# Optimization experiments

Measured on AMD Instinct MI355X. Metric: run time of the kernel, lower is better.

The kernel has to match this reference:

```python
import jax, jax.numpy as jnp
import numpy as np

V, E, Hd, ENC, A = 2000, 256, 256, 256, 256
B, HI, WI, T = 64, 16, 32, 256


def setup_inputs() -> dict:
    key = jax.random.key(0)
    ks = jax.random.split(key, 24)
    n = lambda k, s: jax.random.normal(k, s, dtype=jnp.float32) * 0.05
    return {
        "encoder_out": jax.random.normal(ks[0], (B, ENC, HI, WI), dtype=jnp.float32),
        "captions": jax.random.randint(ks[1], (B, T), 0, V),
        "emb": n(ks[2], (V, E)),
        "W_ae": n(ks[3], (A, ENC)), "b_ae": jnp.zeros((A,), jnp.float32),
        "W_ad": n(ks[4], (A, Hd)), "b_ad": jnp.zeros((A,), jnp.float32),
        "W_fa": n(ks[5], (1, A)), "b_fa": jnp.zeros((1,), jnp.float32),
        "W_inith": n(ks[6], (Hd, ENC)), "b_inith": jnp.zeros((Hd,), jnp.float32),
        "W_initc": n(ks[7], (Hd, ENC)), "b_initc": jnp.zeros((Hd,), jnp.float32),
        "W_ih0": n(ks[8], (4 * Hd, E + ENC)), "W_hh0": n(ks[9], (4 * Hd, Hd)),
        "b_ih0": jnp.zeros((4 * Hd,), jnp.float32), "b_hh0": jnp.zeros((4 * Hd,), jnp.float32),
        "W_ih1": n(ks[10], (4 * Hd, Hd)), "W_hh1": n(ks[11], (4 * Hd, Hd)),
        "b_ih1": jnp.zeros((4 * Hd,), jnp.float32), "b_hh1": jnp.zeros((4 * Hd,), jnp.float32),
        "W_out": n(ks[12], (V, Hd)), "b_out": jnp.zeros((V,), jnp.float32),
    }


def _lstm_cell(x, h, c, Wih, Whh, bih, bhh):
    # PyTorch LSTM gate order: i, f, g, o
    g = x @ Wih.T + h @ Whh.T + bih + bhh
    i, f, gg, o = jnp.split(g, 4, axis=-1)
    c2 = jax.nn.sigmoid(f) * c + jax.nn.sigmoid(i) * jnp.tanh(gg)
    h2 = jax.nn.sigmoid(o) * jnp.tanh(c2)
    return h2, c2


def reference(encoder_out, captions, emb, W_ae, b_ae, W_ad, b_ad, W_fa, b_fa,
              W_inith, b_inith, W_initc, b_initc,
              W_ih0, W_hh0, b_ih0, b_hh0, W_ih1, W_hh1, b_ih1, b_hh1,
              W_out, b_out):
    Bsz, C = encoder_out.shape[0], encoder_out.shape[1]
    enc = encoder_out.reshape(Bsz, C, -1).transpose(0, 2, 1)  # [B, P, C]
    mean = encoder_out.mean(axis=(2, 3))                      # [B, C]
    h0 = jnp.tanh(mean @ W_inith.T + b_inith)
    c0 = jnp.tanh(mean @ W_initc.T + b_initc)
    h = jnp.stack([h0, h0])  # [L, B, Hd]
    c = jnp.stack([c0, c0])
    embs = emb[captions]     # [B, T, E] (dropout disabled / eval)
    att1 = enc @ W_ae.T + b_ae  # [B, P, A], hoisted out of the loop (same math)

    def step(carry, e_t):
        h, c = carry
        att2 = h[-1] @ W_ad.T + b_ad                              # [B, A]
        score = (jnp.tanh(att1 + att2[:, None, :]) @ W_fa.T)[..., 0] + b_fa[0]  # [B, P]
        w = jax.nn.softmax(score, axis=1)
        ctx = jnp.einsum('bp,bpc->bc', w, enc)
        x = jnp.concatenate([e_t, ctx], axis=1)                   # [B, E+C]
        h0n, c0n = _lstm_cell(x, h[0], c[0], W_ih0, W_hh0, b_ih0, b_hh0)
        h1n, c1n = _lstm_cell(h0n, h[1], c[1], W_ih1, W_hh1, b_ih1, b_hh1)
        out_t = h1n @ W_out.T + b_out
        return (jnp.stack([h0n, h1n]), jnp.stack([c0n, c1n])), (out_t, w)

    _, (outs, ws) = jax.lax.scan(step, (h, c), embs.transpose(1, 0, 2))
    return outs.transpose(1, 0, 2), ws.transpose(1, 0, 2)  # [B,T,V], [B,T,P]
```

## Files before the change

### kernel.cpp

```cpp
#include <hip/hip_runtime.h>
#include <math.h>

#define BB 64
#define TT 256
#define VV 2000
#define EE 256
#define HD 256
#define ENC 256
#define AA 256
#define PP 512


typedef unsigned uvec4 __attribute__((ext_vector_type(4)));

__device__ __forceinline__ unsigned short f2h(float f) {
    _Float16 h = (_Float16)f; return __builtin_bit_cast(unsigned short, h);
}
__device__ __forceinline__ void fmlo(float& a, unsigned w, float x) {
    asm("v_fma_mix_f32 %0, %1, %2, %0 op_sel_hi:[1,0,0]" : "+v"(a) : "v"(w), "v"(x));
}
__device__ __forceinline__ void fmhi(float& a, unsigned w, float x) {
    asm("v_fma_mix_f32 %0, %1, %2, %0 op_sel:[1,0,0] op_sel_hi:[1,0,0]" : "+v"(a) : "v"(w), "v"(x));
}
__device__ __forceinline__ void dot8m(float& a0, float& a1, uvec4 w, float4 xa, float4 xb) {
    fmlo(a0, w.x, xa.x); fmhi(a1, w.x, xa.y);
    fmlo(a0, w.y, xa.z); fmhi(a1, w.y, xa.w);
    fmlo(a0, w.z, xb.x); fmhi(a1, w.z, xb.y);
    fmlo(a0, w.w, xb.z); fmhi(a1, w.w, xb.w);
}


__global__ void k_mean(const float* __restrict__ enc, float* __restrict__ meanb) {
    int b = blockIdx.x, c = threadIdx.x;
    const float4* p4 = reinterpret_cast<const float4*>(enc + ((size_t)b*ENC + c)*PP);
    float s = 0.f;
    for (int i = 0; i < PP/4; ++i) { float4 v = p4[i]; s += v.x + v.y + v.z + v.w; }
    meanb[b*ENC + c] = s * (1.0f/PP);
}

__global__ void k_init(const float* __restrict__ meanb,
                       const float* __restrict__ Winith, const float* __restrict__ binith,
                       const float* __restrict__ Winitc, const float* __restrict__ binitc,
                       float* __restrict__ h0, float* __restrict__ c0,
                       float* __restrict__ h1i, float* __restrict__ c1) {
    __shared__ float ms[ENC];
    int b = blockIdx.x, j = threadIdx.x;
    ms[j] = meanb[b*ENC + j];
    __syncthreads();
    float ah = binith[j], ac = binitc[j];
    const float4* wh = (const float4*)(Winith + (size_t)j*ENC);
    const float4* wc = (const float4*)(Winitc + (size_t)j*ENC);
    const float4* m4 = (const float4*)ms;
    for (int k = 0; k < ENC/4; ++k) {
        float4 m = m4[k], a = wh[k], b2 = wc[k];
        ah += a.x*m.x + a.y*m.y + a.z*m.z + a.w*m.w;
        ac += b2.x*m.x + b2.y*m.y + b2.z*m.z + b2.w*m.w;
    }
    float hv = tanhf(ah), cv = tanhf(ac);
    h0[b*HD + j] = hv; c0[b*HD + j] = cv;
    h1i[b*HD + j] = hv; c1[b*HD + j] = cv;
}

__global__ void k_att1T8(const float* __restrict__ enc, const float* __restrict__ Wae,
                         const float* __restrict__ bae, unsigned short* __restrict__ att1T8) {
    __shared__ float wsm[16][ENC];
    int a0 = blockIdx.x * 16, b = blockIdx.y, p = threadIdx.x;
    for (int i = threadIdx.x; i < 16*ENC; i += 512) wsm[i >> 8][i & 255] = Wae[(size_t)a0*ENC + i];
    __syncthreads();
    float acc[16];
    #pragma unroll
    for (int i = 0; i < 16; ++i) acc[i] = 0.f;
    const float* eb = enc + (size_t)b*ENC*PP + p;
    for (int c = 0; c < ENC; ++c) {
        float v = eb[(size_t)c*PP];
        #pragma unroll
        for (int i = 0; i < 16; ++i) acc[i] += v * wsm[i][c];
    }
    #pragma unroll
    for (int q = 0; q < 2; ++q) {
        unsigned short o[8];
        #pragma unroll
        for (int j = 0; j < 8; ++j) o[j] = f2h(acc[q*8+j] + bae[a0 + q*8 + j]);
        *(uint4*)(att1T8 + (((size_t)b*32 + (a0 >> 3) + q)*PP + p)*8) = *(const uint4*)o;
    }
}

__global__ void k_encP(const float* __restrict__ enc, unsigned short* __restrict__ encP) {
    __shared__ float tile[256*33];
    int b = blockIdx.x, p0 = blockIdx.y * 32, tid = threadIdx.x;
    for (int i = tid; i < 256*32; i += 256) {
        int c = i >> 5, pl = i & 31;
        tile[c*33 + pl] = enc[((size_t)b*ENC + c)*PP + p0 + pl];
    }
    __syncthreads();
    for (int j = tid; j < 32*256; j += 256) {
        int p = j >> 8, c = j & 255;
        encP[((size_t)b*PP + p0 + p)*ENC + c] = f2h(tile[c*33 + p]);
    }
}

__global__ void k_cvtT8(const float* __restrict__ src, unsigned short* __restrict__ dst,
                        int nsh, int kc) {
    int i = blockIdx.x*256 + threadIdx.x;
    int N = 1 << nsh;
    int kk = i >> nsh, n = i & (N - 1);
    const float* s = src + (size_t)n*(kc*8) + kk*8;
    unsigned short o[8];
    #pragma unroll
    for (int j = 0; j < 8; ++j) o[j] = f2h(s[j]);
    *(uint4*)(dst + ((size_t)kk*N + n)*8) = *(const uint4*)o;
}


struct KP2 {
    const int* caps; const float* emb;
    const float* Wfa; const float* bfa; const float* bad;
    const float* bih0; const float* bhh0; const float* bih1; const float* bhh1;
    const unsigned short* WadT8;
    const unsigned short* Wih0T8;
    const unsigned short* Whh0T8;
    const unsigned short* Wih1T8;
    const unsigned short* Whh1T8;
    const unsigned short* att1T8;
    const unsigned short* encP;
    const float* h0g; const float* c0g; const float* h1g; const float* c1g;
    float* H1all; float* wsout;
};

__global__ __launch_bounds__(1024, 1) void main64(KP2 P) {
    __shared__ float att2s[AA];
    __shared__ float xt[512];
    __shared__ float h0s[HD], h1s[HD];
    __shared__ float es[PP];
    __shared__ float red[2048];
    __shared__ float bs0[1024], bs1[1024];
    __shared__ float badS[AA], wfaS[AA];
    __shared__ float zinvS, bfaS;
    __shared__ int capS;

    const int b = blockIdx.x, tid = threadIdx.x;

    bs0[tid] = P.bih0[tid] + P.bhh0[tid];
    bs1[tid] = P.bih1[tid] + P.bhh1[tid];
    float c0r = 0.f, c1r = 0.f;
    if (tid < 256) {
        badS[tid] = P.bad[tid]; wfaS[tid] = P.Wfa[tid];
        h0s[tid] = P.h0g[b*HD + tid]; h1s[tid] = P.h1g[b*HD + tid];
        c0r = P.c0g[b*HD + tid];      c1r = P.c1g[b*HD + tid];
    }
    if (tid == 0) bfaS = P.bfa[0];
    __syncthreads();

    const uvec4* att1b = (const uvec4*)(P.att1T8 + (size_t)b*32*PP*8);
    const unsigned* encPb = (const unsigned*)(P.encP + (size_t)b*PP*ENC);
    const uvec4* wadt = (const uvec4*)P.WadT8;
    const uvec4* wi0t = (const uvec4*)P.Wih0T8;
    const uvec4* wh0t = (const uvec4*)P.Whh0T8;
    const uvec4* wi1t = (const uvec4*)P.Wih1T8;
    const uvec4* wh1t = (const uvec4*)P.Whh1T8;

    for (int t = 0; t < TT; ++t) {
        {
            int a = tid & 255, kq = tid >> 8;
            const uvec4* w4 = wadt + (size_t)(kq*8)*256 + a;
            const float4* hv = (const float4*)h1s;
            float a0 = 0.f, a1 = 0.f;
            #pragma unroll
            for (int i = 0; i < 8; ++i) {
                uvec4 w = w4[(size_t)i*256];
                dot8m(a0, a1, w, hv[(kq*8 + i)*2], hv[(kq*8 + i)*2 + 1]);
            }
            red[kq*256 + a] = a0 + a1;
        }
        if (tid == 1023) capS = P.caps[b*TT + t];
        __syncthreads();
        if (tid < 256) att2s[tid] = red[tid] + red[256+tid] + red[512+tid] + red[768+tid] + badS[tid];
        __syncthreads();

        {
            int p = tid & 511, h = tid >> 9;
            const uvec4* a4 = att1b + (size_t)(h*16)*PP + p;
            float sc = 0.f;
            float one = 1.0f;
            #pragma unroll 4
            for (int i = 0; i < 16; ++i) {
                uvec4 w = __builtin_nontemporal_load(a4 + (size_t)i*PP);
                int ab = (h*16 + i)*8;
                #pragma unroll
                for (int j = 0; j < 4; ++j) {
                    unsigned wj = w[j];
                    float a2l = att2s[ab + j*2], a2h = att2s[ab + j*2 + 1];
                    float x0, x1;
                    asm("v_fma_mix_f32 %0, %1, %2, %3 op_sel_hi:[1,0,0]"
                        : "=v"(x0) : "v"(wj), "v"(one), "v"(a2l));
                    asm("v_fma_mix_f32 %0, %1, %2, %3 op_sel:[1,0,0] op_sel_hi:[1,0,0]"
                        : "=v"(x1) : "v"(wj), "v"(one), "v"(a2h));
                    float r0 = __builtin_amdgcn_rcpf(__expf(2.f*x0) + 1.f);
                    float r1 = __builtin_amdgcn_rcpf(__expf(2.f*x1) + 1.f);
                    sc += wfaS[ab + j*2]     * (1.f - 2.f*r0)
                        + wfaS[ab + j*2 + 1] * (1.f - 2.f*r1);
                }
            }
            red[h*512 + p] = sc;
        }
        __syncthreads();
        if (tid < 512) es[tid] = __expf(red[tid] + red[512 + tid] + bfaS);
        __syncthreads();

        if (tid < 64) {
            float z = 0.f;
            #pragma unroll
            for (int i = 0; i < 8; ++i) z += es[tid*8 + i];
            for (int o = 32; o > 0; o >>= 1) z += __shfl_down(z, o, 64);
            if (tid == 0) zinvS = 1.f / z;
        }
        {
            int c2 = tid & 127, pq = tid >> 7;
            float a0 = 0.f, a1 = 0.f;
            #pragma unroll 8
            for (int i = 0; i < 64; ++i) {
                int p = pq*64 + i;
                unsigned w = __builtin_nontemporal_load(encPb + (size_t)p*128 + c2);
                float e = es[p];
                fmlo(a0, w, e); fmhi(a1, w, e);
            }
            red[pq*256 + c2*2]     = a0;
            red[pq*256 + c2*2 + 1] = a1;
        }
        __syncthreads();
        if (tid < 256) {
            float s = 0.f;
            #pragma unroll
            for (int q = 0; q < 8; ++q) s += red[q*256 + tid];
            xt[256 + tid] = s * zinvS;
        } else if (tid < 512) {
            int j = tid - 256;
            xt[j] = P.emb[(size_t)capS*EE + j];
        } else {
            int p = tid - 512;
            P.wsout[((size_t)b*TT + t)*PP + p] = es[p] * zinvS;
        }
        __syncthreads();

        {
            float a0 = bs0[tid], a1 = 0.f;
            const uvec4* wi = wi0t + tid;
            const float4* xv = (const float4*)xt;
            #pragma unroll 8
            for (int kk = 0; kk < 64; ++kk) {
                uvec4 w = wi[(size_t)kk*1024];
                dot8m(a0, a1, w, xv[kk*2], xv[kk*2 + 1]);
            }
            const uvec4* wh = wh0t + tid;
            const float4* hv = (const float4*)h0s;
            #pragma unroll 8
            for (int kk = 0; kk < 32; ++kk) {
                uvec4 w = wh[(size_t)kk*1024];
                dot8m(a0, a1, w, hv[kk*2], hv[kk*2 + 1]);
            }
            red[tid] = a0 + a1;
        }
        __syncthreads();
        if (tid < 256) {
            float gi = red[tid], gf = red[HD+tid], gg = red[2*HD+tid], go = red[3*HD+tid];
            float si = 1.f/(1.f + __expf(-gi)), sf = 1.f/(1.f + __expf(-gf)), so = 1.f/(1.f + __expf(-go));
            c0r = sf*c0r + si*tanhf(gg);
            h0s[tid] = so*tanhf(c0r);
        }
        __syncthreads();

        {
            float a0 = bs1[tid], a1 = 0.f;
            const uvec4* wi = wi1t + tid;
            const float4* hv0 = (const float4*)h0s;
            #pragma unroll 8
            for (int kk = 0; kk < 32; ++kk) {
                uvec4 w = wi[(size_t)kk*1024];
                dot8m(a0, a1, w, hv0[kk*2], hv0[kk*2 + 1]);
            }
            const uvec4* wh = wh1t + tid;
            const float4* hv1 = (const float4*)h1s;
            #pragma unroll 8
            for (int kk = 0; kk < 32; ++kk) {
                uvec4 w = wh[(size_t)kk*1024];
                dot8m(a0, a1, w, hv1[kk*2], hv1[kk*2 + 1]);
            }
            red[tid] = a0 + a1;
        }
        __syncthreads();
        if (tid < 256) {
            float gi = red[tid], gf = red[HD+tid], gg = red[2*HD+tid], go = red[3*HD+tid];
            float si = 1.f/(1.f + __expf(-gi)), sf = 1.f/(1.f + __expf(-gf)), so = 1.f/(1.f + __expf(-go));
            c1r = sf*c1r + si*tanhf(gg);
            float h = so*tanhf(c1r);
            h1s[tid] = h;
            P.H1all[((size_t)t*BB + b)*HD + tid] = h;
        }
        __syncthreads();
    }
}


__global__ __launch_bounds__(256)
void f2_out(const float* __restrict__ H1all, const float* __restrict__ Wout,
            const float* __restrict__ bout, float* __restrict__ out0) {
    __shared__ float Hs[16][260];
    int vt = blockIdx.x, rt = blockIdx.y, tid = threadIdx.x;
    int r0 = rt * 16;
    for (int i = tid; i < 16*256; i += 256) {
        int rl = i >> 8, c = i & 255;
        Hs[rl][c] = H1all[(size_t)(r0 + rl)*HD + c];
    }
    __syncthreads();
    int r_l = tid & 15, v_l = tid >> 4;
    int r = r0 + r_l; int tt = r >> 6, bb2 = r & 63;
    float* orow = out0 + ((size_t)bb2*TT + tt)*VV;
    const float4* hs = (const float4*)Hs[r_l];
    int vbase = vt*128 + v_l*8;
    for (int i = 0; i < 8; ++i) {
        int v = vbase + i;
        if (v >= VV) break;
        const float4* wr = (const float4*)(Wout + (size_t)v*HD);
        float accA = 0.f, accB = 0.f;
        #pragma unroll 4
        for (int k = 0; k < 64; k += 2) {
            float4 w0 = wr[k],   h0 = hs[k];
            float4 w1 = wr[k+1], h1 = hs[k+1];
            accA += w0.x*h0.x + w0.y*h0.y + w0.z*h0.z + w0.w*h0.w;
            accB += w1.x*h1.x + w1.y*h1.y + w1.z*h1.z + w1.w*h1.w;
        }
        orow[v] = accA + accB + bout[v];
    }
}


extern "C" void kernel_launch(void* const* d_in, const int* in_sizes, int n_in,
                              void* d_out, int out_size, void* d_ws, size_t ws_size,
                              hipStream_t stream) {
    const float* enc    = (const float*)d_in[0];
    const int*   caps   = (const int*)  d_in[1];
    const float* emb    = (const float*)d_in[2];
    const float* Wae    = (const float*)d_in[3];
    const float* bae    = (const float*)d_in[4];
    const float* Wad    = (const float*)d_in[5];
    const float* bad    = (const float*)d_in[6];
    const float* Wfa    = (const float*)d_in[7];
    const float* bfa    = (const float*)d_in[8];
    const float* Winith = (const float*)d_in[9];
    const float* binith = (const float*)d_in[10];
    const float* Winitc = (const float*)d_in[11];
    const float* binitc = (const float*)d_in[12];
    const float* Wih0   = (const float*)d_in[13];
    const float* Whh0   = (const float*)d_in[14];
    const float* bih0   = (const float*)d_in[15];
    const float* bhh0   = (const float*)d_in[16];
    const float* Wih1   = (const float*)d_in[17];
    const float* Whh1   = (const float*)d_in[18];
    const float* bih1   = (const float*)d_in[19];
    const float* bhh1   = (const float*)d_in[20];
    const float* Wout   = (const float*)d_in[21];
    const float* bout   = (const float*)d_in[22];

    float* ws = (float*)d_ws;
    unsigned short* att1T8 = (unsigned short*)(ws);
    unsigned short* encP   = (unsigned short*)(ws + 4194304);
    float* H1all = ws + 8388608;
    unsigned short* Wih0T8 = (unsigned short*)(ws + 12582912);
    unsigned short* Whh0T8 = (unsigned short*)(ws + 12845056);
    unsigned short* Wih1T8 = (unsigned short*)(ws + 12976128);
    unsigned short* Whh1T8 = (unsigned short*)(ws + 13107200);
    unsigned short* WadT8  = (unsigned short*)(ws + 13238272);
    float* meanb = ws + 13271040;
    float* h0g   = ws + 13287424;
    float* c0g   = ws + 13303808;
    float* h1g   = ws + 13320192;
    float* c1g   = ws + 13336576;

    float* out0  = (float*)d_out;
    float* wsout = out0 + (size_t)BB*TT*VV;

    hipLaunchKernelGGL(k_mean,   dim3(BB),     dim3(256), 0, stream, enc, meanb);
    hipLaunchKernelGGL(k_init,   dim3(BB),     dim3(256), 0, stream, meanb, Winith, binith,
                       Winitc, binitc, h0g, c0g, h1g, c1g);
    hipLaunchKernelGGL(k_att1T8, dim3(16, BB), dim3(512), 0, stream, enc, Wae, bae, att1T8);
    hipLaunchKernelGGL(k_encP,   dim3(BB, 16), dim3(256), 0, stream, enc, encP);
    hipLaunchKernelGGL(k_cvtT8,  dim3(256),    dim3(256), 0, stream, Wih0, Wih0T8, 10, 64);
    hipLaunchKernelGGL(k_cvtT8,  dim3(128),    dim3(256), 0, stream, Whh0, Whh0T8, 10, 32);
    hipLaunchKernelGGL(k_cvtT8,  dim3(128),    dim3(256), 0, stream, Wih1, Wih1T8, 10, 32);
    hipLaunchKernelGGL(k_cvtT8,  dim3(128),    dim3(256), 0, stream, Whh1, Whh1T8, 10, 32);
    hipLaunchKernelGGL(k_cvtT8,  dim3(32),     dim3(256), 0, stream, Wad,  WadT8,   8, 32);

    KP2 kp;
    kp.caps = caps; kp.emb = emb;
    kp.Wfa = Wfa; kp.bfa = bfa; kp.bad = bad;
    kp.bih0 = bih0; kp.bhh0 = bhh0; kp.bih1 = bih1; kp.bhh1 = bhh1;
    kp.WadT8 = WadT8; kp.Wih0T8 = Wih0T8; kp.Whh0T8 = Whh0T8; kp.Wih1T8 = Wih1T8; kp.Whh1T8 = Whh1T8;
    kp.att1T8 = att1T8; kp.encP = encP;
    kp.h0g = h0g; kp.c0g = c0g; kp.h1g = h1g; kp.c1g = c1g;
    kp.H1all = H1all; kp.wsout = wsout;

    hipLaunchKernelGGL(main64, dim3(BB), dim3(1024), 0, stream, kp);

    hipLaunchKernelGGL(f2_out, dim3(16, 1024), dim3(256), 0, stream, H1all, Wout, bout, out0);
}
```

Before: 11.91 ms.

## Keep att1 in registers, fold tanh scales into weights, use exp2 activations

The per-batch att1 slice is loaded once into 16 vector registers per thread, so each timestep no longer re-streams it from global memory. The tanh in the attention score is rewritten algebraically: the 2*log2(e) factor is prescaled into att1, Wad and bad, the sum of Wfa is hoisted, and each element then needs only exp2, rcp and one FMA. LSTM sigmoid and tanh now use raw exp2/rcp intrinsics, and the embedding fetch moves earlier to overlap with the att2 phase. The cost is much higher register pressure (64 extra VGPRs at 1024 threads) and slightly different rounding, since the prescaled values are stored in fp16.

```diff
diff --git a/kernel.cpp b/kernel.cpp
--- a/kernel.cpp
+++ b/kernel.cpp
@@ -10,6 +10,9 @@
 #define AA 256
 #define PP 512
 
+#define S2L 2.8853900817779268f
+#define SL  1.4426950408889634f
+
 
 typedef unsigned uvec4 __attribute__((ext_vector_type(4)));
 
@@ -27,6 +30,14 @@
     fmlo(a0, w.y, xa.z); fmhi(a1, w.y, xa.w);
     fmlo(a0, w.z, xb.x); fmhi(a1, w.z, xb.y);
     fmlo(a0, w.w, xb.z); fmhi(a1, w.w, xb.w);
+}
+__device__ __forceinline__ float ftanh(float x) {
+    float u = __builtin_amdgcn_exp2f(x * S2L);
+    return 1.f - 2.f * __builtin_amdgcn_rcpf(u + 1.f);
+}
+__device__ __forceinline__ float fsigm(float x) {
+    float u = __builtin_amdgcn_exp2f(x * SL);
+    return u * __builtin_amdgcn_rcpf(u + 1.f);
 }
 
 
@@ -80,7 +91,7 @@
     for (int q = 0; q < 2; ++q) {
         unsigned short o[8];
         #pragma unroll
-        for (int j = 0; j < 8; ++j) o[j] = f2h(acc[q*8+j] + bae[a0 + q*8 + j]);
+        for (int j = 0; j < 8; ++j) o[j] = f2h((acc[q*8+j] + bae[a0 + q*8 + j]) * S2L);
         *(uint4*)(att1T8 + (((size_t)b*32 + (a0 >> 3) + q)*PP + p)*8) = *(const uint4*)o;
     }
 }
@@ -100,14 +111,14 @@
 }
 
 __global__ void k_cvtT8(const float* __restrict__ src, unsigned short* __restrict__ dst,
-                        int nsh, int kc) {
+                        int nsh, int kc, float scale) {
     int i = blockIdx.x*256 + threadIdx.x;
     int N = 1 << nsh;
     int kk = i >> nsh, n = i & (N - 1);
     const float* s = src + (size_t)n*(kc*8) + kk*8;
     unsigned short o[8];
     #pragma unroll
-    for (int j = 0; j < 8; ++j) o[j] = f2h(s[j]);
+    for (int j = 0; j < 8; ++j) o[j] = f2h(s[j] * scale);
     *(uint4*)(dst + ((size_t)kk*N + n)*8) = *(const uint4*)o;
 }
 
@@ -135,8 +146,7 @@
     __shared__ float red[2048];
     __shared__ float bs0[1024], bs1[1024];
     __shared__ float badS[AA], wfaS[AA];
-    __shared__ float zinvS, bfaS;
-    __shared__ int capS;
+    __shared__ float zinvS, bfaS, wfaSumS;
 
     const int b = blockIdx.x, tid = threadIdx.x;
 
@@ -144,20 +154,34 @@
     bs1[tid] = P.bih1[tid] + P.bhh1[tid];
     float c0r = 0.f, c1r = 0.f;
     if (tid < 256) {
-        badS[tid] = P.bad[tid]; wfaS[tid] = P.Wfa[tid];
+        badS[tid] = P.bad[tid] * S2L;
+        wfaS[tid] = P.Wfa[tid] * SL;
         h0s[tid] = P.h0g[b*HD + tid]; h1s[tid] = P.h1g[b*HD + tid];
         c0r = P.c0g[b*HD + tid];      c1r = P.c1g[b*HD + tid];
     }
-    if (tid == 0) bfaS = P.bfa[0];
-    __syncthreads();
-
-    const uvec4* att1b = (const uvec4*)(P.att1T8 + (size_t)b*32*PP*8);
+    if (tid == 0) bfaS = P.bfa[0] * SL;
+    __syncthreads();
+    if (tid == 0) {
+        float s = 0.f;
+        for (int i = 0; i < 256; ++i) s += wfaS[i];
+        wfaSumS = s;
+    }
+
+    const int p_sc = tid & 511, h_sc = tid >> 9;
+    uvec4 aw[16];
+    {
+        const uvec4* a4 = (const uvec4*)(P.att1T8 + (size_t)b*32*PP*8) + (size_t)(h_sc*16)*PP + p_sc;
+        #pragma unroll
+        for (int i = 0; i < 16; ++i) aw[i] = a4[(size_t)i*PP];
+    }
+
     const unsigned* encPb = (const unsigned*)(P.encP + (size_t)b*PP*ENC);
     const uvec4* wadt = (const uvec4*)P.WadT8;
     const uvec4* wi0t = (const uvec4*)P.Wih0T8;
     const uvec4* wh0t = (const uvec4*)P.Whh0T8;
     const uvec4* wi1t = (const uvec4*)P.Wih1T8;
     const uvec4* wh1t = (const uvec4*)P.Whh1T8;
+    __syncthreads();
 
     for (int t = 0; t < TT; ++t) {
         {
@@ -172,39 +196,40 @@
             }
             red[kq*256 + a] = a0 + a1;
         }
-        if (tid == 1023) capS = P.caps[b*TT + t];
+        if (tid < 256) {
+            int cap = P.caps[b*TT + t];
+            xt[tid] = P.emb[(size_t)cap*EE + tid];
+        }
         __syncthreads();
         if (tid < 256) att2s[tid] = red[tid] + red[256+tid] + red[512+tid] + red[768+tid] + badS[tid];
         __syncthreads();
 
         {
-            int p = tid & 511, h = tid >> 9;
-            const uvec4* a4 = att1b + (size_t)(h*16)*PP + p;
-            float sc = 0.f;
-            float one = 1.0f;
+            float partial = 0.f;
             #pragma unroll 4
             for (int i = 0; i < 16; ++i) {
-                uvec4 w = __builtin_nontemporal_load(a4 + (size_t)i*PP);
-                int ab = (h*16 + i)*8;
+                uvec4 w = aw[i];
+                int ab = (h_sc*16 + i)*8;
                 #pragma unroll
                 for (int j = 0; j < 4; ++j) {
                     unsigned wj = w[j];
                     float a2l = att2s[ab + j*2], a2h = att2s[ab + j*2 + 1];
                     float x0, x1;
                     asm("v_fma_mix_f32 %0, %1, %2, %3 op_sel_hi:[1,0,0]"
-                        : "=v"(x0) : "v"(wj), "v"(one), "v"(a2l));
+                        : "=v"(x0) : "v"(wj), "v"(1.0f), "v"(a2l));
                     asm("v_fma_mix_f32 %0, %1, %2, %3 op_sel:[1,0,0] op_sel_hi:[1,0,0]"
-                        : "=v"(x1) : "v"(wj), "v"(one), "v"(a2h));
-                    float r0 = __builtin_amdgcn_rcpf(__expf(2.f*x0) + 1.f);
-                    float r1 = __builtin_amdgcn_rcpf(__expf(2.f*x1) + 1.f);
-                    sc += wfaS[ab + j*2]     * (1.f - 2.f*r0)
-                        + wfaS[ab + j*2 + 1] * (1.f - 2.f*r1);
+                        : "=v"(x1) : "v"(wj), "v"(1.0f), "v"(a2h));
+                    float r0 = __builtin_amdgcn_rcpf(__builtin_amdgcn_exp2f(x0) + 1.f);
+                    float r1 = __builtin_amdgcn_rcpf(__builtin_amdgcn_exp2f(x1) + 1.f);
+                    partial = fmaf(wfaS[ab + j*2],     r0, partial);
+                    partial = fmaf(wfaS[ab + j*2 + 1], r1, partial);
                 }
             }
-            red[h*512 + p] = sc;
-        }
-        __syncthreads();
-        if (tid < 512) es[tid] = __expf(red[tid] + red[512 + tid] + bfaS);
+            red[h_sc*512 + p_sc] = partial;
+        }
+        __syncthreads();
+        if (tid < 512)
+            es[tid] = __builtin_amdgcn_exp2f(wfaSumS - 2.f*(red[tid] + red[512 + tid]) + bfaS);
         __syncthreads();
 
         if (tid < 64) {
@@ -233,10 +258,7 @@
             #pragma unroll
             for (int q = 0; q < 8; ++q) s += red[q*256 + tid];
             xt[256 + tid] = s * zinvS;
-        } else if (tid < 512) {
-            int j = tid - 256;
-            xt[j] = P.emb[(size_t)capS*EE + j];
-        } else {
+        } else if (tid >= 512) {
             int p = tid - 512;
             P.wsout[((size_t)b*TT + t)*PP + p] = es[p] * zinvS;
         }
@@ -263,9 +285,8 @@
         __syncthreads();
         if (tid < 256) {
             float gi = red[tid], gf = red[HD+tid], gg = red[2*HD+tid], go = red[3*HD+tid];
-            float si = 1.f/(1.f + __expf(-gi)), sf = 1.f/(1.f + __expf(-gf)), so = 1.f/(1.f + __expf(-go));
-            c0r = sf*c0r + si*tanhf(gg);
-            h0s[tid] = so*tanhf(c0r);
+            c0r = fsigm(gf)*c0r + fsigm(gi)*ftanh(gg);
+            h0s[tid] = fsigm(go)*ftanh(c0r);
         }
         __syncthreads();
 
@@ -290,9 +311,8 @@
         __syncthreads();
         if (tid < 256) {
             float gi = red[tid], gf = red[HD+tid], gg = red[2*HD+tid], go = red[3*HD+tid];
-            float si = 1.f/(1.f + __expf(-gi)), sf = 1.f/(1.f + __expf(-gf)), so = 1.f/(1.f + __expf(-go));
-            c1r = sf*c1r + si*tanhf(gg);
-            float h = so*tanhf(c1r);
+            c1r = fsigm(gf)*c1r + fsigm(gi)*ftanh(gg);
+            float h = fsigm(go)*ftanh(c1r);
             h1s[tid] = h;
             P.H1all[((size_t)t*BB + b)*HD + tid] = h;
         }
@@ -384,11 +404,11 @@
                        Winitc, binitc, h0g, c0g, h1g, c1g);
     hipLaunchKernelGGL(k_att1T8, dim3(16, BB), dim3(512), 0, stream, enc, Wae, bae, att1T8);
     hipLaunchKernelGGL(k_encP,   dim3(BB, 16), dim3(256), 0, stream, enc, encP);
-    hipLaunchKernelGGL(k_cvtT8,  dim3(256),    dim3(256), 0, stream, Wih0, Wih0T8, 10, 64);
-    hipLaunchKernelGGL(k_cvtT8,  dim3(128),    dim3(256), 0, stream, Whh0, Whh0T8, 10, 32);
-    hipLaunchKernelGGL(k_cvtT8,  dim3(128),    dim3(256), 0, stream, Wih1, Wih1T8, 10, 32);
-    hipLaunchKernelGGL(k_cvtT8,  dim3(128),    dim3(256), 0, stream, Whh1, Whh1T8, 10, 32);
-    hipLaunchKernelGGL(k_cvtT8,  dim3(32),     dim3(256), 0, stream, Wad,  WadT8,   8, 32);
+    hipLaunchKernelGGL(k_cvtT8,  dim3(256),    dim3(256), 0, stream, Wih0, Wih0T8, 10, 64, 1.0f);
+    hipLaunchKernelGGL(k_cvtT8,  dim3(128),    dim3(256), 0, stream, Whh0, Whh0T8, 10, 32, 1.0f);
+    hipLaunchKernelGGL(k_cvtT8,  dim3(128),    dim3(256), 0, stream, Wih1, Wih1T8, 10, 32, 1.0f);
+    hipLaunchKernelGGL(k_cvtT8,  dim3(128),    dim3(256), 0, stream, Whh1, Whh1T8, 10, 32, 1.0f);
+    hipLaunchKernelGGL(k_cvtT8,  dim3(32),     dim3(256), 0, stream, Wad,  WadT8,   8, 32, S2L);
 
     KP2 kp;
     kp.caps = caps; kp.emb = emb;
```

Measured after the change: 18.10 ms. 52.0% more time.
